# Kernel optimization log

Measured on AMD Instinct MI355X. Metric: run time of the kernel, lower is better.

## Reference

```python
import jax, jax.numpy as jnp
import numpy as np

B, NMAX, H, DH, K = 16, 1024, 4, 32, 16
C = H * DH  # 128 = hidden_dim
T = 8192


def _dense_batch(feat, batch):
    # PyG to_dense_batch: [T, ...] + segment ids -> [B, NMAX, ...] + mask
    t = feat.shape[0]
    counts = jax.ops.segment_sum(jnp.ones((t,), jnp.int32), batch, num_segments=B)
    starts = jnp.concatenate([jnp.zeros((1,), jnp.int32), jnp.cumsum(counts)[:-1].astype(jnp.int32)])
    idx = jnp.arange(t) - starts[batch]
    dense = jnp.zeros((B, NMAX) + feat.shape[1:], feat.dtype).at[batch, idx].set(feat)
    mask = jnp.zeros((B, NMAX), bool).at[batch, idx].set(True)
    return dense, mask


def _forward(batch, x, pos, emb_W, emb_b, Wq, Wk, Wv0, Wv1, Wo0, Wo1, Wg, dist_scale, head_W, head_b):
    # 1) node embedding, then dense-batch (as in original forward)
    f0_flat = x @ emb_W + emb_b                      # [T, C]
    f0, mask = _dense_batch(f0_flat, batch)          # [B,N,C], [B,N]
    coords, _ = _dense_batch(pos, batch)             # [B,N,3]

    # 2) kNN graph from coordinates (num_neighbors=16, attend_self=True -> self is nearest)
    rel = coords[:, :, None, :] - coords[:, None, :, :]      # [B,N,N,3]
    d2 = jnp.sum(rel * rel, axis=-1)                         # [B,N,N]
    pv = mask[:, :, None] & mask[:, None, :]
    d2m = jnp.where(pv, d2, 1e9)
    _, nbr = jax.lax.top_k(-d2m, K)                          # [B,N,K]

    bidx = jnp.arange(B)[:, None, None]
    rel_n = jnp.take_along_axis(rel, nbr[..., None], axis=2)  # [B,N,K,3]
    d2_n = jnp.take_along_axis(d2, nbr, axis=2)               # [B,N,K]
    nbr_valid = jnp.take_along_axis(pv, nbr, axis=2)          # [B,N,K]
    dist = jnp.sqrt(d2_n + 1e-6)
    direc = rel_n / dist[..., None]                           # degree-1 spherical harmonic (unit rel dir)

    # 3) SE(3)-equivariant kNN attention (degree-0 and degree-1 outputs)
    q = (f0 @ Wq).reshape(B, NMAX, H, DH)
    k_n = (f0 @ Wk)[bidx, nbr].reshape(B, NMAX, K, H, DH)
    v0_n = (f0 @ Wv0)[bidx, nbr].reshape(B, NMAX, K, H, DH)
    v1_n = (f0 @ Wv1)[bidx, nbr].reshape(B, NMAX, K, H, DH)

    logits = jnp.einsum('bnhd,bnkhd->bnhk', q, k_n) / np.sqrt(DH)
    logits = logits - jax.nn.softplus(dist_scale)[None, None, :, None] * dist[:, :, None, :]
    logits = jnp.where(nbr_valid[:, :, None, :], logits, -1e9)
    attn = jax.nn.softmax(logits, axis=-1)                    # [B,N,H,K]

    out0 = jnp.einsum('bnhk,bnkhd->bnhd', attn, v0_n).reshape(B, NMAX, C)
    out1 = jnp.einsum('bnhk,bnkhd,bnkj->bnhdj', attn, v1_n, direc).reshape(B, NMAX, C, 3)

    # equivariant channel mixing of type-1, then invariant norm gates type-0 (residual)
    f1 = jnp.einsum('bncj,cd->bndj', out1, Wo1)               # [B,N,C,3]
    inv = jnp.sqrt(jnp.sum(f1 * f1, axis=-1) + 1e-6)          # [B,N,C]
    f0_out = f0 + out0 @ Wo0 + inv @ Wg

    # 4) masked mean pool over nodes + linear head
    mf = mask.astype(f0_out.dtype)
    pooled = jnp.sum(f0_out * mf[..., None], axis=1) / jnp.maximum(jnp.sum(mf, axis=1, keepdims=True), 1.0)
    return pooled @ head_W + head_b                           # [B, 19]


def setup_inputs() -> dict:
    key = jax.random.key(0)
    ks = jax.random.split(key, 16)
    def w(k, shape, fan_in):
        return jax.random.normal(k, shape, jnp.float32) / np.sqrt(fan_in)
    return {
        'x': jax.random.normal(ks[0], (T, 11), jnp.float32),
        'pos': jax.random.normal(ks[1], (T, 3), jnp.float32),
        'batch': jnp.sort(jax.random.randint(ks[2], (T,), 0, B)),
        'emb_W': w(ks[3], (11, C), 11), 'emb_b': jnp.zeros((C,), jnp.float32),
        'Wq': w(ks[4], (C, C), C), 'Wk': w(ks[5], (C, C), C),
        'Wv0': w(ks[6], (C, C), C), 'Wv1': w(ks[7], (C, C), C),
        'Wo0': w(ks[8], (C, C), C), 'Wo1': w(ks[9], (C, C), C),
        'Wg': w(ks[10], (C, C), C),
        'dist_scale': jax.random.normal(ks[11], (H,), jnp.float32) * 0.1,
        'head_W': w(ks[12], (C, 19), C), 'head_b': jnp.zeros((19,), jnp.float32),
    }


def reference(x, pos, batch, emb_W, emb_b, Wq, Wk, Wv0, Wv1, Wo0, Wo1, Wg, dist_scale, head_W, head_b):
    return _forward(batch, x, pos, emb_W, emb_b, Wq, Wk, Wv0, Wv1, Wo0, Wo1, Wg, dist_scale, head_W, head_b)
```

## Files before the change

### kernel.cpp

```cpp
#include <hip/hip_runtime.h>
#include <hip/hip_bf16.h>
#include <math.h>

#define T_NODES 8192
#define BGRAPHS 16
#define CDIM 128
#define HEADS 4
#define DHEAD 32
#define KNN 16

template <int NS>
__device__ __forceinline__ void knn_body(const float* __restrict__ pos,
                                         int t, int s, int n, int lane,
                                         float px, float py, float pz,
                                         int* __restrict__ nbr,
                                         float4* __restrict__ dird) {
    float sd[NS];
    int ss[NS];
#pragma unroll
    for (int sl = 0; sl < NS; ++sl) {
        int j = lane + sl * 64;
        float d2 = 1e30f;
        if (j < n) {
            int jj = s + j;
            float dx = px - pos[jj * 3 + 0];
            float dy = py - pos[jj * 3 + 1];
            float dz = pz - pos[jj * 3 + 2];
            d2 = dx * dx + dy * dy + dz * dz;
        }
        sd[sl] = d2;
        ss[sl] = sl;
    }

#pragma unroll
    for (int p = 1; p < NS; p <<= 1) {
#pragma unroll
        for (int k = p; k >= 1; k >>= 1) {
#pragma unroll
            for (int j = (k & (p - 1)); j + k < NS; j += 2 * k) {
#pragma unroll
                for (int i = 0; i < k; ++i) {
                    if (i + j + k < NS && ((i + j) / (2 * p)) == ((i + j + k) / (2 * p))) {
                        int a = i + j, c2 = i + j + k;
                        bool sw = sd[a] > sd[c2];
                        float td = sd[a];
                        int ts = ss[a];
                        sd[a] = sw ? sd[c2] : sd[a];
                        ss[a] = sw ? ss[c2] : ss[a];
                        sd[c2] = sw ? td : sd[c2];
                        ss[c2] = sw ? ts : ss[c2];
                    }
                }
            }
        }
    }

    float resd = 1e30f;
    int resj = -1;

#pragma unroll
    for (int r = 0; r < KNN; ++r) {
        float rd = sd[0];
#pragma unroll
        for (int off = 32; off >= 1; off >>= 1) {
            rd = fminf(rd, __shfl_xor(rd, off));
        }
        unsigned long long mask = __ballot(sd[0] == rd);
        int wl = (int)__builtin_ctzll(mask);
        int ws = __shfl(ss[0], wl);
        if (lane == r) { resd = rd; resj = wl + ws * 64; }
        if (lane == wl) {
#pragma unroll
            for (int i = 0; i < NS - 1; ++i) { sd[i] = sd[i + 1]; ss[i] = ss[i + 1]; }
            sd[NS - 1] = 1e30f;
        }
    }

    if (lane < KNN) {
        bool valid = (resd < 1e29f);
        int jf = valid ? (s + resj) : -1;
        nbr[t * KNN + lane] = jf;
        float dd = sqrtf(resd + 1e-6f);
        float dx = 0.f, dy = 0.f, dz = 0.f;
        if (valid) {
            float inv = 1.f / dd;
            dx = (px - pos[jf * 3 + 0]) * inv;
            dy = (py - pos[jf * 3 + 1]) * inv;
            dz = (pz - pos[jf * 3 + 2]) * inv;
        }
        float4 v;
        v.x = dx; v.y = dy; v.z = dz; v.w = dd;
        dird[t * KNN + lane] = v;
    }
}

__global__ __launch_bounds__(256) void k_par(const float* __restrict__ pos,
                                             const int* __restrict__ batch,
                                             const float* __restrict__ x,
                                             const float* __restrict__ embW,
                                             const float* __restrict__ embb,
                                             const float* __restrict__ Wq,
                                             const float* __restrict__ Wk,
                                             const float* __restrict__ Wv0,
                                             const float* __restrict__ Wv1,
                                             const float* __restrict__ Wo0,
                                             const float* __restrict__ Wg,
                                             const float* __restrict__ headW,
                                             int* __restrict__ nbr,
                                             float4* __restrict__ dird,
                                             float* __restrict__ f0,
                                             float* __restrict__ qkvv,
                                             float* __restrict__ H1,
                                             float* __restrict__ H2) {
    __shared__ float smem[CDIM * 20];
    int bid = blockIdx.x;
    int tid = threadIdx.x;

    if (bid >= 2560) {
        int m = bid - 2560;
        const float* W = m ? Wg : Wo0;
        float* H = m ? H2 : H1;
        for (int i = tid; i < CDIM * 19; i += 256) smem[i] = headW[i];
        __syncthreads();
        for (int i = tid; i < CDIM * 19; i += 256) {
            int c = i / 19, o = i - c * 19;
            float acc = 0.f;
#pragma unroll 8
            for (int d = 0; d < CDIM; ++d) acc += W[c * CDIM + d] * smem[d * 19 + o];
            H[i] = acc;
        }
        return;
    }

    int g = bid / 5, r = bid - g * 5;
    if (r == 4) {
        float (*sf)[CDIM] = (float (*)[CDIM])smem;
        int t0 = g * 16;
        {
            int col = tid & 127;
            int pr = tid >> 7;
            float ew[11];
#pragma unroll
            for (int i = 0; i < 11; ++i) ew[i] = embW[i * CDIM + col];
            float eb = embb[col];
#pragma unroll
            for (int nn8 = 0; nn8 < 8; ++nn8) {
                int nn = pr * 8 + nn8;
                int t = t0 + nn;
                float acc = eb;
#pragma unroll
                for (int i = 0; i < 11; ++i) acc += x[t * 11 + i] * ew[i];
                sf[nn][col] = acc;
                f0[(size_t)t * CDIM + col] = acc;
            }
        }
        __syncthreads();

        const float* W1 = (tid < 128) ? Wq : Wk;
        const float* W2 = (tid < 128) ? Wv0 : Wv1;
        int col = tid & 127;

        float acc1[16], acc2[16];
#pragma unroll
        for (int nn = 0; nn < 16; ++nn) { acc1[nn] = 0.f; acc2[nn] = 0.f; }

        for (int c0 = 0; c0 < CDIM; c0 += 8) {
            float w1[8], w2[8];
#pragma unroll
            for (int cc = 0; cc < 8; ++cc) {
                w1[cc] = W1[(c0 + cc) * CDIM + col];
                w2[cc] = W2[(c0 + cc) * CDIM + col];
            }
#pragma unroll
            for (int nn = 0; nn < 16; ++nn) {
                float4 fa = *(const float4*)&sf[nn][c0];
                float4 fb = *(const float4*)&sf[nn][c0 + 4];
                acc1[nn] += fa.x * w1[0] + fa.y * w1[1] + fa.z * w1[2] + fa.w * w1[3]
                          + fb.x * w1[4] + fb.y * w1[5] + fb.z * w1[6] + fb.w * w1[7];
                acc2[nn] += fa.x * w2[0] + fa.y * w2[1] + fa.z * w2[2] + fa.w * w2[3]
                          + fb.x * w2[4] + fb.y * w2[5] + fb.z * w2[6] + fb.w * w2[7];
            }
        }
#pragma unroll
        for (int nn = 0; nn < 16; ++nn) {
            qkvv[(size_t)(t0 + nn) * 512 + tid] = acc1[nn];
            qkvv[(size_t)(t0 + nn) * 512 + 256 + tid] = acc2[nn];
        }
        return;
    }

    int kidx = g * 4 + r;
    int wave = tid >> 6;
    int lane = tid & 63;
    int t = kidx * 4 + wave;

    int b = batch[t];

    int pb = t - lane * 16;
    int qf = t + lane * 16;
    int vb = batch[pb < 0 ? 0 : pb];
    int vf = batch[qf > T_NODES - 1 ? T_NODES - 1 : qf];
    bool eqb = (pb >= 0) && (vb == b);
    bool eqf = (qf < T_NODES) && (vf == b);
    unsigned long long mb = __ballot(eqb);
    unsigned long long mf = __ballot(eqf);
    int m1 = (~mb == 0ULL) ? 64 : (int)__builtin_ctzll(~mb);
    int m2 = (~mf == 0ULL) ? 64 : (int)__builtin_ctzll(~mf);
    int wsb = (m1 == 64) ? (t - 1023) : (t - m1 * 16 + 1);
    int wsf = (m2 == 64) ? (t + 1009) : (t + (m2 - 1) * 16 + 1);
    int pos2 = (lane < 16) ? (wsb + lane) : (wsf + (lane - 16));
    int pc = pos2 < 0 ? 0 : (pos2 > T_NODES - 1 ? T_NODES - 1 : pos2);
    int v2 = batch[pc];
    bool cb = (lane < 16) && ((pos2 < 0) || (v2 < b));
    bool cf = (lane >= 16) && (lane < 32) && (pos2 < T_NODES) && (v2 == b);
    int s = wsb + (int)__popcll(__ballot(cb));
    int e = wsf + (int)__popcll(__ballot(cf));
    int n = e - s;

    float px = pos[t * 3 + 0];
    float py = pos[t * 3 + 1];
    float pz = pos[t * 3 + 2];

    if (n <= 512) {
        knn_body<8>(pos, t, s, n, lane, px, py, pz, nbr, dird);
    } else {
        knn_body<16>(pos, t, s, n, lane, px, py, pz, nbr, dird);
    }
}

__global__ __launch_bounds__(256) void k_attn(const float* __restrict__ qkvv,
                                              const int* __restrict__ nbr,
                                              const float4* __restrict__ dird,
                                              const float* __restrict__ dist_scale,
                                              const float* __restrict__ Wo1,
                                              float* __restrict__ out0,
                                              float* __restrict__ invb) {
    __shared__ float  s_a[4][64];
    __shared__ float4 s_d[4][16];
    __shared__ int    s_j[4][16];
    __shared__ float  s_o1[4][CDIM][4];
    __shared__ float  s_part[CDIM][13];

    int bid = blockIdx.x;
    int swz = (bid & 7) * (T_NODES / 32) + (bid >> 3);
    int wave = threadIdx.x >> 6;
    int lane = threadIdx.x & 63;
    int t = swz * 4 + wave;

    int k = lane & 15;
    int h = lane >> 4;

    int j = nbr[t * KNN + k];
    float4 dv = dird[t * KNN + k];
    if (h == 0) { s_j[wave][k] = j; s_d[wave][k] = dv; }

    const float4* qv = (const float4*)&qkvv[(size_t)t * 512 + h * DHEAD];
    const float4* kv = (j >= 0) ? (const float4*)&qkvv[(size_t)j * 512 + 128 + h * DHEAD] : qv;
    float dot = 0.f;
#pragma unroll
    for (int i = 0; i < 8; ++i) {
        float4 a = qv[i], b2 = kv[i];
        dot += a.x * b2.x + a.y * b2.y + a.z * b2.z + a.w * b2.w;
    }
    float xs = dist_scale[h];
    float sp = (xs > 20.f) ? xs : log1pf(expf(xs));
    float lg = (j >= 0) ? (dot * 0.17677669529663687f - sp * dv.w) : -1e30f;

    float m = lg;
    m = fmaxf(m, __shfl_xor(m, 1));
    m = fmaxf(m, __shfl_xor(m, 2));
    m = fmaxf(m, __shfl_xor(m, 4));
    m = fmaxf(m, __shfl_xor(m, 8));
    float e = expf(lg - m);
    float ssum = e;
    ssum += __shfl_xor(ssum, 1);
    ssum += __shfl_xor(ssum, 2);
    ssum += __shfl_xor(ssum, 4);
    ssum += __shfl_xor(ssum, 8);
    s_a[wave][h * 16 + k] = e / ssum;

    __syncthreads();

    int c2 = lane * 2;
    int hh = lane >> 4;

    float o0x = 0.f, o0y = 0.f;
    float o1xx = 0.f, o1xy = 0.f;
    float o1yx = 0.f, o1yy = 0.f;
    float o1zx = 0.f, o1zy = 0.f;

#pragma unroll
    for (int kk = 0; kk < KNN; ++kk) {
        int jj = s_j[wave][kk];
        if (jj >= 0) {
            float a = s_a[wave][hh * 16 + kk];
            float4 d = s_d[wave][kk];
            float2 v0 = *(const float2*)&qkvv[(size_t)jj * 512 + 256 + c2];
            float2 v1 = *(const float2*)&qkvv[(size_t)jj * 512 + 384 + c2];
            o0x += a * v0.x;
            o0y += a * v0.y;
            float w1x = a * v1.x, w1y = a * v1.y;
            o1xx += w1x * d.x; o1xy += w1y * d.x;
            o1yx += w1x * d.y; o1yy += w1y * d.y;
            o1zx += w1x * d.z; o1zy += w1y * d.z;
        }
    }

    float2 st;
    st.x = o0x; st.y = o0y;
    *(float2*)&out0[(size_t)t * CDIM + c2] = st;

    {
        float4 w0; w0.x = o1xx; w0.y = o1yx; w0.z = o1zx; w0.w = 0.f;
        float4 w1; w1.x = o1xy; w1.y = o1yy; w1.z = o1zy; w1.w = 0.f;
        *(float4*)&s_o1[wave][c2][0] = w0;
        *(float4*)&s_o1[wave][c2 + 1][0] = w1;
    }
    __syncthreads();

    int d = threadIdx.x & 127;
    int half = threadIdx.x >> 7;
    int t0 = swz * 4;

    float acc[4][3];
#pragma unroll
    for (int nn = 0; nn < 4; ++nn) { acc[nn][0] = 0.f; acc[nn][1] = 0.f; acc[nn][2] = 0.f; }

    int cb0 = half * 64;
#pragma unroll 4
    for (int c = cb0; c < cb0 + 64; ++c) {
        float wv = Wo1[c * CDIM + d];
#pragma unroll
        for (int nn = 0; nn < 4; ++nn) {
            float4 v = *(const float4*)&s_o1[nn][c][0];
            acc[nn][0] += v.x * wv;
            acc[nn][1] += v.y * wv;
            acc[nn][2] += v.z * wv;
        }
    }
    if (half == 1) {
#pragma unroll
        for (int nn = 0; nn < 4; ++nn) {
            s_part[d][nn * 3 + 0] = acc[nn][0];
            s_part[d][nn * 3 + 1] = acc[nn][1];
            s_part[d][nn * 3 + 2] = acc[nn][2];
        }
    }
    __syncthreads();
    if (half == 0) {
#pragma unroll
        for (int nn = 0; nn < 4; ++nn) {
            float fx = acc[nn][0] + s_part[d][nn * 3 + 0];
            float fy = acc[nn][1] + s_part[d][nn * 3 + 1];
            float fz = acc[nn][2] + s_part[d][nn * 3 + 2];
            invb[(size_t)(t0 + nn) * CDIM + d] = sqrtf(fx * fx + fy * fy + fz * fz + 1e-6f);
        }
    }
}

__global__ __launch_bounds__(1024) void k_pool(const float* __restrict__ f0,
                                               const float* __restrict__ out0,
                                               const float* __restrict__ invb,
                                               const int* __restrict__ batch,
                                               const float* __restrict__ headW,
                                               const float* __restrict__ H1,
                                               const float* __restrict__ H2,
                                               const float* __restrict__ headb,
                                               float* __restrict__ out) {
    __shared__ float p0[8][CDIM], p1[8][CDIM], p2[8][CDIM];
    int b = blockIdx.x;
    int tid = threadIdx.x;
    int c = tid & 127;
    int slice = tid >> 7;

    int lo = 0, hi = T_NODES;
    while (lo < hi) {
        int mid = (lo + hi) >> 1;
        bool lt = batch[mid] < b;
        lo = lt ? mid + 1 : lo;
        hi = lt ? hi : mid;
    }
    int s = lo;
    lo = 0; hi = T_NODES;
    while (lo < hi) {
        int mid = (lo + hi) >> 1;
        bool le = batch[mid] <= b;
        lo = le ? mid + 1 : lo;
        hi = le ? hi : mid;
    }
    int n = lo - s;

    float a0 = 0.f, a1 = 0.f, a2 = 0.f;
    for (int i = slice; i < n; i += 8) {
        size_t idx = (size_t)(s + i) * CDIM + c;
        a0 += f0[idx];
        a1 += out0[idx];
        a2 += invb[idx];
    }
    p0[slice][c] = a0;
    p1[slice][c] = a1;
    p2[slice][c] = a2;
    __syncthreads();

    if (slice == 0) {
        float inv_n = 1.f / fmaxf((float)n, 1.f);
        float v0 = p0[0][c] + p0[1][c] + p0[2][c] + p0[3][c]
                 + p0[4][c] + p0[5][c] + p0[6][c] + p0[7][c];
        float v1 = p1[0][c] + p1[1][c] + p1[2][c] + p1[3][c]
                 + p1[4][c] + p1[5][c] + p1[6][c] + p1[7][c];
        float v2 = p2[0][c] + p2[1][c] + p2[2][c] + p2[3][c]
                 + p2[4][c] + p2[5][c] + p2[6][c] + p2[7][c];
        p0[0][c] = v0 * inv_n;
        p1[0][c] = v1 * inv_n;
        p2[0][c] = v2 * inv_n;
    }
    __syncthreads();

    if (tid < 19 * 32) {
        int o = tid >> 5;
        int l = tid & 31;
        float p = 0.f;
#pragma unroll
        for (int cc = 0; cc < 4; ++cc) {
            int ch = l + cc * 32;
            p += p0[0][ch] * headW[ch * 19 + o]
               + p1[0][ch] * H1[ch * 19 + o]
               + p2[0][ch] * H2[ch * 19 + o];
        }
        p += __shfl_xor(p, 16);
        p += __shfl_xor(p, 8);
        p += __shfl_xor(p, 4);
        p += __shfl_xor(p, 2);
        p += __shfl_xor(p, 1);
        if (l == 0) out[b * 19 + o] = p + headb[o];
    }
}

extern "C" void kernel_launch(void* const* d_in, const int* in_sizes, int n_in,
                              void* d_out, int out_size, void* d_ws, size_t ws_size,
                              hipStream_t stream) {
    const float* x    = (const float*)d_in[0];
    const float* pos  = (const float*)d_in[1];
    const int* batch  = (const int*)d_in[2];
    const float* embW = (const float*)d_in[3];
    const float* embb = (const float*)d_in[4];
    const float* Wq   = (const float*)d_in[5];
    const float* Wk   = (const float*)d_in[6];
    const float* Wv0  = (const float*)d_in[7];
    const float* Wv1  = (const float*)d_in[8];
    const float* Wo0  = (const float*)d_in[9];
    const float* Wo1  = (const float*)d_in[10];
    const float* Wg   = (const float*)d_in[11];
    const float* dist_scale = (const float*)d_in[12];
    const float* headW = (const float*)d_in[13];
    const float* headb = (const float*)d_in[14];
    float* out = (float*)d_out;

    char* w = (char*)d_ws;
    float* f0   = (float*)(w + 256);
    float* qkvv = f0 + (size_t)T_NODES * CDIM;
    int* nbr    = (int*)(qkvv + (size_t)T_NODES * 512);
    float4* dird = (float4*)(nbr + (size_t)T_NODES * KNN);
    float* out0 = (float*)(dird + (size_t)T_NODES * KNN);
    float* invb = out0 + (size_t)T_NODES * CDIM;
    float* H1   = invb + (size_t)T_NODES * CDIM;
    float* H2   = H1 + CDIM * 19;

    k_par<<<2562, 256, 0, stream>>>(pos, batch, x, embW, embb, Wq, Wk, Wv0, Wv1,
                                    Wo0, Wg, headW, nbr, dird, f0, qkvv, H1, H2);
    k_attn<<<T_NODES / 4, 256, 0, stream>>>(qkvv, nbr, dird, dist_scale, Wo1, out0, invb);
    k_pool<<<BGRAPHS, 1024, 0, stream>>>(f0, out0, invb, batch, headW, H1, H2, headb, out);
}
```

Measured before the change: 134.6 us.

## Fuse mean pooling into producers via atomics and pair kNN queries per wave

The per-node f0, out0 and invb arrays are no longer written to global memory. The embedding stage and the attention kernel now accumulate per-graph sums with run-length grouped atomicAdds into small pooled buffers, zeroed by a memset, and the pool kernel only scales and applies the head. The kNN stage now handles two query nodes per wave, using 32-lane halves with a packed-key min reduction when both segments have at most 512 nodes, which cuts the kNN block count. This removes several megabytes of global traffic and the pool kernel's serial reduction, but adds atomic contention, a memset launch, and float summation order that is no longer deterministic.

Result: faster. 113.2 us (-15.9%).

```diff
diff --git a/kernel.cpp b/kernel.cpp
--- a/kernel.cpp
+++ b/kernel.cpp
@@ -9,193 +9,9 @@
 #define DHEAD 32
 #define KNN 16
 
-template <int NS>
-__device__ __forceinline__ void knn_body(const float* __restrict__ pos,
-                                         int t, int s, int n, int lane,
-                                         float px, float py, float pz,
-                                         int* __restrict__ nbr,
-                                         float4* __restrict__ dird) {
-    float sd[NS];
-    int ss[NS];
-#pragma unroll
-    for (int sl = 0; sl < NS; ++sl) {
-        int j = lane + sl * 64;
-        float d2 = 1e30f;
-        if (j < n) {
-            int jj = s + j;
-            float dx = px - pos[jj * 3 + 0];
-            float dy = py - pos[jj * 3 + 1];
-            float dz = pz - pos[jj * 3 + 2];
-            d2 = dx * dx + dy * dy + dz * dz;
-        }
-        sd[sl] = d2;
-        ss[sl] = sl;
-    }
-
-#pragma unroll
-    for (int p = 1; p < NS; p <<= 1) {
-#pragma unroll
-        for (int k = p; k >= 1; k >>= 1) {
-#pragma unroll
-            for (int j = (k & (p - 1)); j + k < NS; j += 2 * k) {
-#pragma unroll
-                for (int i = 0; i < k; ++i) {
-                    if (i + j + k < NS && ((i + j) / (2 * p)) == ((i + j + k) / (2 * p))) {
-                        int a = i + j, c2 = i + j + k;
-                        bool sw = sd[a] > sd[c2];
-                        float td = sd[a];
-                        int ts = ss[a];
-                        sd[a] = sw ? sd[c2] : sd[a];
-                        ss[a] = sw ? ss[c2] : ss[a];
-                        sd[c2] = sw ? td : sd[c2];
-                        ss[c2] = sw ? ts : ss[c2];
-                    }
-                }
-            }
-        }
-    }
-
-    float resd = 1e30f;
-    int resj = -1;
-
-#pragma unroll
-    for (int r = 0; r < KNN; ++r) {
-        float rd = sd[0];
-#pragma unroll
-        for (int off = 32; off >= 1; off >>= 1) {
-            rd = fminf(rd, __shfl_xor(rd, off));
-        }
-        unsigned long long mask = __ballot(sd[0] == rd);
-        int wl = (int)__builtin_ctzll(mask);
-        int ws = __shfl(ss[0], wl);
-        if (lane == r) { resd = rd; resj = wl + ws * 64; }
-        if (lane == wl) {
-#pragma unroll
-            for (int i = 0; i < NS - 1; ++i) { sd[i] = sd[i + 1]; ss[i] = ss[i + 1]; }
-            sd[NS - 1] = 1e30f;
-        }
-    }
-
-    if (lane < KNN) {
-        bool valid = (resd < 1e29f);
-        int jf = valid ? (s + resj) : -1;
-        nbr[t * KNN + lane] = jf;
-        float dd = sqrtf(resd + 1e-6f);
-        float dx = 0.f, dy = 0.f, dz = 0.f;
-        if (valid) {
-            float inv = 1.f / dd;
-            dx = (px - pos[jf * 3 + 0]) * inv;
-            dy = (py - pos[jf * 3 + 1]) * inv;
-            dz = (pz - pos[jf * 3 + 2]) * inv;
-        }
-        float4 v;
-        v.x = dx; v.y = dy; v.z = dz; v.w = dd;
-        dird[t * KNN + lane] = v;
-    }
-}
-
-__global__ __launch_bounds__(256) void k_par(const float* __restrict__ pos,
-                                             const int* __restrict__ batch,
-                                             const float* __restrict__ x,
-                                             const float* __restrict__ embW,
-                                             const float* __restrict__ embb,
-                                             const float* __restrict__ Wq,
-                                             const float* __restrict__ Wk,
-                                             const float* __restrict__ Wv0,
-                                             const float* __restrict__ Wv1,
-                                             const float* __restrict__ Wo0,
-                                             const float* __restrict__ Wg,
-                                             const float* __restrict__ headW,
-                                             int* __restrict__ nbr,
-                                             float4* __restrict__ dird,
-                                             float* __restrict__ f0,
-                                             float* __restrict__ qkvv,
-                                             float* __restrict__ H1,
-                                             float* __restrict__ H2) {
-    __shared__ float smem[CDIM * 20];
-    int bid = blockIdx.x;
-    int tid = threadIdx.x;
-
-    if (bid >= 2560) {
-        int m = bid - 2560;
-        const float* W = m ? Wg : Wo0;
-        float* H = m ? H2 : H1;
-        for (int i = tid; i < CDIM * 19; i += 256) smem[i] = headW[i];
-        __syncthreads();
-        for (int i = tid; i < CDIM * 19; i += 256) {
-            int c = i / 19, o = i - c * 19;
-            float acc = 0.f;
-#pragma unroll 8
-            for (int d = 0; d < CDIM; ++d) acc += W[c * CDIM + d] * smem[d * 19 + o];
-            H[i] = acc;
-        }
-        return;
-    }
-
-    int g = bid / 5, r = bid - g * 5;
-    if (r == 4) {
-        float (*sf)[CDIM] = (float (*)[CDIM])smem;
-        int t0 = g * 16;
-        {
-            int col = tid & 127;
-            int pr = tid >> 7;
-            float ew[11];
-#pragma unroll
-            for (int i = 0; i < 11; ++i) ew[i] = embW[i * CDIM + col];
-            float eb = embb[col];
-#pragma unroll
-            for (int nn8 = 0; nn8 < 8; ++nn8) {
-                int nn = pr * 8 + nn8;
-                int t = t0 + nn;
-                float acc = eb;
-#pragma unroll
-                for (int i = 0; i < 11; ++i) acc += x[t * 11 + i] * ew[i];
-                sf[nn][col] = acc;
-                f0[(size_t)t * CDIM + col] = acc;
-            }
-        }
-        __syncthreads();
-
-        const float* W1 = (tid < 128) ? Wq : Wk;
-        const float* W2 = (tid < 128) ? Wv0 : Wv1;
-        int col = tid & 127;
-
-        float acc1[16], acc2[16];
-#pragma unroll
-        for (int nn = 0; nn < 16; ++nn) { acc1[nn] = 0.f; acc2[nn] = 0.f; }
-
-        for (int c0 = 0; c0 < CDIM; c0 += 8) {
-            float w1[8], w2[8];
-#pragma unroll
-            for (int cc = 0; cc < 8; ++cc) {
-                w1[cc] = W1[(c0 + cc) * CDIM + col];
-                w2[cc] = W2[(c0 + cc) * CDIM + col];
-            }
-#pragma unroll
-            for (int nn = 0; nn < 16; ++nn) {
-                float4 fa = *(const float4*)&sf[nn][c0];
-                float4 fb = *(const float4*)&sf[nn][c0 + 4];
-                acc1[nn] += fa.x * w1[0] + fa.y * w1[1] + fa.z * w1[2] + fa.w * w1[3]
-                          + fb.x * w1[4] + fb.y * w1[5] + fb.z * w1[6] + fb.w * w1[7];
-                acc2[nn] += fa.x * w2[0] + fa.y * w2[1] + fa.z * w2[2] + fa.w * w2[3]
-                          + fb.x * w2[4] + fb.y * w2[5] + fb.z * w2[6] + fb.w * w2[7];
-            }
-        }
-#pragma unroll
-        for (int nn = 0; nn < 16; ++nn) {
-            qkvv[(size_t)(t0 + nn) * 512 + tid] = acc1[nn];
-            qkvv[(size_t)(t0 + nn) * 512 + 256 + tid] = acc2[nn];
-        }
-        return;
-    }
-
-    int kidx = g * 4 + r;
-    int wave = tid >> 6;
-    int lane = tid & 63;
-    int t = kidx * 4 + wave;
-
+__device__ __forceinline__ void seg_probe(const int* __restrict__ batch, int t,
+                                          int lane, int& s_out, int& n_out) {
     int b = batch[t];
-
     int pb = t - lane * 16;
     int qf = t + lane * 16;
     int vb = batch[pb < 0 ? 0 : pb];
@@ -213,39 +29,328 @@
     int v2 = batch[pc];
     bool cb = (lane < 16) && ((pos2 < 0) || (v2 < b));
     bool cf = (lane >= 16) && (lane < 32) && (pos2 < T_NODES) && (v2 == b);
-    int s = wsb + (int)__popcll(__ballot(cb));
-    int e = wsf + (int)__popcll(__ballot(cf));
-    int n = e - s;
-
-    float px = pos[t * 3 + 0];
-    float py = pos[t * 3 + 1];
-    float pz = pos[t * 3 + 2];
-
-    if (n <= 512) {
-        knn_body<8>(pos, t, s, n, lane, px, py, pz, nbr, dird);
+    s_out = wsb + (int)__popcll(__ballot(cb));
+    n_out = wsf + (int)__popcll(__ballot(cf)) - s_out;
+}
+
+template <int NS>
+__device__ __forceinline__ void knn_body(const float* __restrict__ pos,
+                                         int t, int s, int n, int lane,
+                                         int* __restrict__ nbr,
+                                         float4* __restrict__ dird) {
+    float px = pos[t * 3 + 0], py = pos[t * 3 + 1], pz = pos[t * 3 + 2];
+    float sd[NS];
+    int ss[NS];
+#pragma unroll
+    for (int sl = 0; sl < NS; ++sl) {
+        int j = lane + sl * 64;
+        float d2 = 1e30f;
+        if (j < n) {
+            int jj = s + j;
+            float dx = px - pos[jj * 3 + 0];
+            float dy = py - pos[jj * 3 + 1];
+            float dz = pz - pos[jj * 3 + 2];
+            d2 = dx * dx + dy * dy + dz * dz;
+        }
+        sd[sl] = d2;
+        ss[sl] = sl;
+    }
+#pragma unroll
+    for (int p = 1; p < NS; p <<= 1) {
+#pragma unroll
+        for (int k = p; k >= 1; k >>= 1) {
+#pragma unroll
+            for (int j = (k & (p - 1)); j + k < NS; j += 2 * k) {
+#pragma unroll
+                for (int i = 0; i < k; ++i) {
+                    if (i + j + k < NS && ((i + j) / (2 * p)) == ((i + j + k) / (2 * p))) {
+                        int a = i + j, c2 = i + j + k;
+                        bool sw = sd[a] > sd[c2];
+                        float td = sd[a];
+                        int ts = ss[a];
+                        sd[a] = sw ? sd[c2] : sd[a];
+                        ss[a] = sw ? ss[c2] : ss[a];
+                        sd[c2] = sw ? td : sd[c2];
+                        ss[c2] = sw ? ts : ss[c2];
+                    }
+                }
+            }
+        }
+    }
+
+    float resd = 1e30f;
+    int resj = -1;
+#pragma unroll
+    for (int r = 0; r < KNN; ++r) {
+        float rd = sd[0];
+#pragma unroll
+        for (int off = 32; off >= 1; off >>= 1) {
+            rd = fminf(rd, __shfl_xor(rd, off));
+        }
+        unsigned long long mask = __ballot(sd[0] == rd);
+        int wl = (int)__builtin_ctzll(mask);
+        int ws = __shfl(ss[0], wl);
+        if (lane == r) { resd = rd; resj = wl + ws * 64; }
+        if (lane == wl) {
+#pragma unroll
+            for (int i = 0; i < NS - 1; ++i) { sd[i] = sd[i + 1]; ss[i] = ss[i + 1]; }
+            sd[NS - 1] = 1e30f;
+        }
+    }
+
+    if (lane < KNN) {
+        bool valid = (resd < 1e29f);
+        int jf = valid ? (s + resj) : -1;
+        nbr[t * KNN + lane] = jf;
+        float dd = sqrtf(resd + 1e-6f);
+        float dx = 0.f, dy = 0.f, dz = 0.f;
+        if (valid) {
+            float inv = 1.f / dd;
+            dx = (px - pos[jf * 3 + 0]) * inv;
+            dy = (py - pos[jf * 3 + 1]) * inv;
+            dz = (pz - pos[jf * 3 + 2]) * inv;
+        }
+        float4 v;
+        v.x = dx; v.y = dy; v.z = dz; v.w = dd;
+        dird[t * KNN + lane] = v;
+    }
+}
+
+template <int NS>
+__device__ __forceinline__ void knn_pair_body(const float* __restrict__ pos,
+                                              int t, int s, int n, int lane,
+                                              int* __restrict__ nbr,
+                                              float4* __restrict__ dird) {
+    int l32 = lane & 31;
+    float px = pos[t * 3 + 0], py = pos[t * 3 + 1], pz = pos[t * 3 + 2];
+    float sd[NS];
+    int ss[NS];
+#pragma unroll
+    for (int sl = 0; sl < NS; ++sl) {
+        int j = l32 + sl * 32;
+        float d2 = 1e30f;
+        if (j < n) {
+            int jj = s + j;
+            float dx = px - pos[jj * 3 + 0];
+            float dy = py - pos[jj * 3 + 1];
+            float dz = pz - pos[jj * 3 + 2];
+            d2 = dx * dx + dy * dy + dz * dz;
+        }
+        sd[sl] = d2;
+        ss[sl] = sl;
+    }
+#pragma unroll
+    for (int p = 1; p < NS; p <<= 1) {
+#pragma unroll
+        for (int k = p; k >= 1; k >>= 1) {
+#pragma unroll
+            for (int j = (k & (p - 1)); j + k < NS; j += 2 * k) {
+#pragma unroll
+                for (int i = 0; i < k; ++i) {
+                    if (i + j + k < NS && ((i + j) / (2 * p)) == ((i + j + k) / (2 * p))) {
+                        int a = i + j, c2 = i + j + k;
+                        bool sw = sd[a] > sd[c2];
+                        float td = sd[a];
+                        int ts = ss[a];
+                        sd[a] = sw ? sd[c2] : sd[a];
+                        ss[a] = sw ? ss[c2] : ss[a];
+                        sd[c2] = sw ? td : sd[c2];
+                        ss[c2] = sw ? ts : ss[c2];
+                    }
+                }
+            }
+        }
+    }
+
+    float resd = 1e30f;
+    int resj = -1;
+#pragma unroll
+    for (int r = 0; r < KNN; ++r) {
+        unsigned key = (__float_as_uint(sd[0]) & ~31u) | (unsigned)l32;
+        key = min(key, (unsigned)__shfl_xor((int)key, 16));
+        key = min(key, (unsigned)__shfl_xor((int)key, 8));
+        key = min(key, (unsigned)__shfl_xor((int)key, 4));
+        key = min(key, (unsigned)__shfl_xor((int)key, 2));
+        key = min(key, (unsigned)__shfl_xor((int)key, 1));
+        int wl32 = (int)(key & 31u);
+        int wl = wl32 + (lane & 32);
+        float rd = __shfl(sd[0], wl);
+        int ws = __shfl(ss[0], wl);
+        if (l32 == r) { resd = rd; resj = wl32 + ws * 32; }
+        if (lane == wl) {
+#pragma unroll
+            for (int i = 0; i < NS - 1; ++i) { sd[i] = sd[i + 1]; ss[i] = ss[i + 1]; }
+            sd[NS - 1] = 1e30f;
+        }
+    }
+
+    if (l32 < KNN) {
+        bool valid = (resd < 1e29f);
+        int jf = valid ? (s + resj) : -1;
+        nbr[t * KNN + l32] = jf;
+        float dd = sqrtf(resd + 1e-6f);
+        float dx = 0.f, dy = 0.f, dz = 0.f;
+        if (valid) {
+            float inv = 1.f / dd;
+            dx = (px - pos[jf * 3 + 0]) * inv;
+            dy = (py - pos[jf * 3 + 1]) * inv;
+            dz = (pz - pos[jf * 3 + 2]) * inv;
+        }
+        float4 v;
+        v.x = dx; v.y = dy; v.z = dz; v.w = dd;
+        dird[t * KNN + l32] = v;
+    }
+}
+
+__global__ __launch_bounds__(256) void k_par(const float* __restrict__ pos,
+                                             const int* __restrict__ batch,
+                                             const float* __restrict__ x,
+                                             const float* __restrict__ embW,
+                                             const float* __restrict__ embb,
+                                             const float* __restrict__ Wq,
+                                             const float* __restrict__ Wk,
+                                             const float* __restrict__ Wv0,
+                                             const float* __restrict__ Wv1,
+                                             const float* __restrict__ Wo0,
+                                             const float* __restrict__ Wg,
+                                             const float* __restrict__ headW,
+                                             int* __restrict__ nbr,
+                                             float4* __restrict__ dird,
+                                             float* __restrict__ qkvv,
+                                             float* __restrict__ poolF0,
+                                             float* __restrict__ H1,
+                                             float* __restrict__ H2) {
+    __shared__ float smem[CDIM * 20];
+    int bid = blockIdx.x;
+    int tid = threadIdx.x;
+
+    if (bid >= 1536) {
+        int m = bid - 1536;
+        const float* W = m ? Wg : Wo0;
+        float* H = m ? H2 : H1;
+        for (int i = tid; i < CDIM * 19; i += 256) smem[i] = headW[i];
+        __syncthreads();
+        for (int i = tid; i < CDIM * 19; i += 256) {
+            int c = i / 19, o = i - c * 19;
+            float acc = 0.f;
+#pragma unroll 8
+            for (int d = 0; d < CDIM; ++d) acc += W[c * CDIM + d] * smem[d * 19 + o];
+            H[i] = acc;
+        }
+        return;
+    }
+
+    int g = bid / 3, r = bid - g * 3;
+    if (r == 2) {
+        float (*sf)[CDIM] = (float (*)[CDIM])smem;
+        int t0 = g * 16;
+        {
+            int col = tid & 127;
+            int pr = tid >> 7;
+            float ew[11];
+#pragma unroll
+            for (int i = 0; i < 11; ++i) ew[i] = embW[i * CDIM + col];
+            float eb = embb[col];
+            float acc_run = 0.f;
+            int gprev = batch[t0 + pr * 8];
+#pragma unroll
+            for (int nn8 = 0; nn8 < 8; ++nn8) {
+                int nn = pr * 8 + nn8;
+                int t = t0 + nn;
+                float acc = eb;
+#pragma unroll
+                for (int i = 0; i < 11; ++i) acc += x[t * 11 + i] * ew[i];
+                sf[nn][col] = acc;
+                int gb = batch[t];
+                if (gb != gprev) {
+                    atomicAdd(&poolF0[gprev * CDIM + col], acc_run);
+                    acc_run = 0.f;
+                    gprev = gb;
+                }
+                acc_run += acc;
+            }
+            atomicAdd(&poolF0[gprev * CDIM + col], acc_run);
+        }
+        __syncthreads();
+
+        const float* W1 = (tid < 128) ? Wq : Wk;
+        const float* W2 = (tid < 128) ? Wv0 : Wv1;
+        int col = tid & 127;
+
+        float acc1[16], acc2[16];
+#pragma unroll
+        for (int nn = 0; nn < 16; ++nn) { acc1[nn] = 0.f; acc2[nn] = 0.f; }
+
+        for (int c0 = 0; c0 < CDIM; c0 += 8) {
+            float w1[8], w2[8];
+#pragma unroll
+            for (int cc = 0; cc < 8; ++cc) {
+                w1[cc] = W1[(c0 + cc) * CDIM + col];
+                w2[cc] = W2[(c0 + cc) * CDIM + col];
+            }
+#pragma unroll
+            for (int nn = 0; nn < 16; ++nn) {
+                float4 fa = *(const float4*)&sf[nn][c0];
+                float4 fb = *(const float4*)&sf[nn][c0 + 4];
+                acc1[nn] += fa.x * w1[0] + fa.y * w1[1] + fa.z * w1[2] + fa.w * w1[3]
+                          + fb.x * w1[4] + fb.y * w1[5] + fb.z * w1[6] + fb.w * w1[7];
+                acc2[nn] += fa.x * w2[0] + fa.y * w2[1] + fa.z * w2[2] + fa.w * w2[3]
+                          + fb.x * w2[4] + fb.y * w2[5] + fb.z * w2[6] + fb.w * w2[7];
+            }
+        }
+#pragma unroll
+        for (int nn = 0; nn < 16; ++nn) {
+            qkvv[(size_t)(t0 + nn) * 512 + tid] = acc1[nn];
+            qkvv[(size_t)(t0 + nn) * 512 + 256 + tid] = acc2[nn];
+        }
+        return;
+    }
+
+    int kidx = g * 2 + r;
+    int wave = tid >> 6;
+    int lane = tid & 63;
+    int tA = kidx * 8 + wave * 2;
+    int tB = tA + 1;
+
+    int sA, nA, sB, nB;
+    seg_probe(batch, tA, lane, sA, nA);
+    seg_probe(batch, tB, lane, sB, nB);
+
+    int nmax = nA > nB ? nA : nB;
+    if (nmax <= 512) {
+        int t = (lane < 32) ? tA : tB;
+        int s = (lane < 32) ? sA : sB;
+        int n = (lane < 32) ? nA : nB;
+        knn_pair_body<16>(pos, t, s, n, lane, nbr, dird);
     } else {
-        knn_body<16>(pos, t, s, n, lane, px, py, pz, nbr, dird);
+        knn_body<16>(pos, tA, sA, nA, lane, nbr, dird);
+        knn_body<16>(pos, tB, sB, nB, lane, nbr, dird);
     }
 }
 
 __global__ __launch_bounds__(256) void k_attn(const float* __restrict__ qkvv,
                                               const int* __restrict__ nbr,
                                               const float4* __restrict__ dird,
+                                              const int* __restrict__ batch,
                                               const float* __restrict__ dist_scale,
                                               const float* __restrict__ Wo1,
-                                              float* __restrict__ out0,
-                                              float* __restrict__ invb) {
+                                              float* __restrict__ poolO0,
+                                              float* __restrict__ poolInv) {
     __shared__ float  s_a[4][64];
     __shared__ float4 s_d[4][16];
     __shared__ int    s_j[4][16];
     __shared__ float  s_o1[4][CDIM][4];
     __shared__ float  s_part[CDIM][13];
+    __shared__ int    s_gid[4];
 
     int bid = blockIdx.x;
     int swz = (bid & 7) * (T_NODES / 32) + (bid >> 3);
     int wave = threadIdx.x >> 6;
     int lane = threadIdx.x & 63;
-    int t = swz * 4 + wave;
+    int t0 = swz * 4;
+    int t = t0 + wave;
+
+    if (threadIdx.x < 4) s_gid[threadIdx.x] = batch[t0 + threadIdx.x];
 
     int k = lane & 15;
     int h = lane >> 4;
@@ -306,13 +411,9 @@
         }
     }
 
-    float2 st;
-    st.x = o0x; st.y = o0y;
-    *(float2*)&out0[(size_t)t * CDIM + c2] = st;
-
     {
-        float4 w0; w0.x = o1xx; w0.y = o1yx; w0.z = o1zx; w0.w = 0.f;
-        float4 w1; w1.x = o1xy; w1.y = o1yy; w1.z = o1zy; w1.w = 0.f;
+        float4 w0; w0.x = o1xx; w0.y = o1yx; w0.z = o1zx; w0.w = o0x;
+        float4 w1; w1.x = o1xy; w1.y = o1yy; w1.z = o1zy; w1.w = o0y;
         *(float4*)&s_o1[wave][c2][0] = w0;
         *(float4*)&s_o1[wave][c2 + 1][0] = w1;
     }
@@ -320,7 +421,6 @@
 
     int d = threadIdx.x & 127;
     int half = threadIdx.x >> 7;
-    int t0 = swz * 4;
 
     float acc[4][3];
 #pragma unroll
@@ -348,30 +448,42 @@
     }
     __syncthreads();
     if (half == 0) {
+        float accO = 0.f, accI = 0.f;
+        int gprev = s_gid[0];
 #pragma unroll
         for (int nn = 0; nn < 4; ++nn) {
             float fx = acc[nn][0] + s_part[d][nn * 3 + 0];
             float fy = acc[nn][1] + s_part[d][nn * 3 + 1];
             float fz = acc[nn][2] + s_part[d][nn * 3 + 2];
-            invb[(size_t)(t0 + nn) * CDIM + d] = sqrtf(fx * fx + fy * fy + fz * fz + 1e-6f);
-        }
-    }
-}
-
-__global__ __launch_bounds__(1024) void k_pool(const float* __restrict__ f0,
-                                               const float* __restrict__ out0,
-                                               const float* __restrict__ invb,
-                                               const int* __restrict__ batch,
-                                               const float* __restrict__ headW,
-                                               const float* __restrict__ H1,
-                                               const float* __restrict__ H2,
-                                               const float* __restrict__ headb,
-                                               float* __restrict__ out) {
-    __shared__ float p0[8][CDIM], p1[8][CDIM], p2[8][CDIM];
+            float iv = sqrtf(fx * fx + fy * fy + fz * fz + 1e-6f);
+            float o0v = s_o1[nn][d][3];
+            int gb = s_gid[nn];
+            if (gb != gprev) {
+                atomicAdd(&poolO0[gprev * CDIM + d], accO);
+                atomicAdd(&poolInv[gprev * CDIM + d], accI);
+                accO = 0.f; accI = 0.f;
+                gprev = gb;
+            }
+            accO += o0v;
+            accI += iv;
+        }
+        atomicAdd(&poolO0[gprev * CDIM + d], accO);
+        atomicAdd(&poolInv[gprev * CDIM + d], accI);
+    }
+}
+
+__global__ __launch_bounds__(640) void k_pool(const float* __restrict__ poolF0,
+                                              const float* __restrict__ poolO0,
+                                              const float* __restrict__ poolInv,
+                                              const int* __restrict__ batch,
+                                              const float* __restrict__ headW,
+                                              const float* __restrict__ H1,
+                                              const float* __restrict__ H2,
+                                              const float* __restrict__ headb,
+                                              float* __restrict__ out) {
+    __shared__ float P0[CDIM], P1[CDIM], P2[CDIM];
     int b = blockIdx.x;
     int tid = threadIdx.x;
-    int c = tid & 127;
-    int slice = tid >> 7;
 
     int lo = 0, hi = T_NODES;
     while (lo < hi) {
@@ -389,30 +501,12 @@
         hi = le ? hi : mid;
     }
     int n = lo - s;
-
-    float a0 = 0.f, a1 = 0.f, a2 = 0.f;
-    for (int i = slice; i < n; i += 8) {
-        size_t idx = (size_t)(s + i) * CDIM + c;
-        a0 += f0[idx];
-        a1 += out0[idx];
-        a2 += invb[idx];
-    }
-    p0[slice][c] = a0;
-    p1[slice][c] = a1;
-    p2[slice][c] = a2;
-    __syncthreads();
-
-    if (slice == 0) {
-        float inv_n = 1.f / fmaxf((float)n, 1.f);
-        float v0 = p0[0][c] + p0[1][c] + p0[2][c] + p0[3][c]
-                 + p0[4][c] + p0[5][c] + p0[6][c] + p0[7][c];
-        float v1 = p1[0][c] + p1[1][c] + p1[2][c] + p1[3][c]
-                 + p1[4][c] + p1[5][c] + p1[6][c] + p1[7][c];
-        float v2 = p2[0][c] + p2[1][c] + p2[2][c] + p2[3][c]
-                 + p2[4][c] + p2[5][c] + p2[6][c] + p2[7][c];
-        p0[0][c] = v0 * inv_n;
-        p1[0][c] = v1 * inv_n;
-        p2[0][c] = v2 * inv_n;
+    float inv_n = 1.f / fmaxf((float)n, 1.f);
+
+    if (tid < CDIM) {
+        P0[tid] = poolF0[b * CDIM + tid] * inv_n;
+        P1[tid] = poolO0[b * CDIM + tid] * inv_n;
+        P2[tid] = poolInv[b * CDIM + tid] * inv_n;
     }
     __syncthreads();
 
@@ -423,9 +517,9 @@
 #pragma unroll
         for (int cc = 0; cc < 4; ++cc) {
             int ch = l + cc * 32;
-            p += p0[0][ch] * headW[ch * 19 + o]
-               + p1[0][ch] * H1[ch * 19 + o]
-               + p2[0][ch] * H2[ch * 19 + o];
+            p += P0[ch] * headW[ch * 19 + o]
+               + P1[ch] * H1[ch * 19 + o]
+               + P2[ch] * H2[ch * 19 + o];
         }
         p += __shfl_xor(p, 16);
         p += __shfl_xor(p, 8);
@@ -457,17 +551,20 @@
     float* out = (float*)d_out;
 
     char* w = (char*)d_ws;
-    float* f0   = (float*)(w + 256);
-    float* qkvv = f0 + (size_t)T_NODES * CDIM;
+    float* qkvv = (float*)(w + 256);
     int* nbr    = (int*)(qkvv + (size_t)T_NODES * 512);
     float4* dird = (float4*)(nbr + (size_t)T_NODES * KNN);
-    float* out0 = (float*)(dird + (size_t)T_NODES * KNN);
-    float* invb = out0 + (size_t)T_NODES * CDIM;
-    float* H1   = invb + (size_t)T_NODES * CDIM;
+    float* poolF0 = (float*)(dird + (size_t)T_NODES * KNN);
+    float* poolO0 = poolF0 + BGRAPHS * CDIM;
+    float* poolInv = poolO0 + BGRAPHS * CDIM;
+    float* H1   = poolInv + BGRAPHS * CDIM;
     float* H2   = H1 + CDIM * 19;
 
-    k_par<<<2562, 256, 0, stream>>>(pos, batch, x, embW, embb, Wq, Wk, Wv0, Wv1,
-                                    Wo0, Wg, headW, nbr, dird, f0, qkvv, H1, H2);
-    k_attn<<<T_NODES / 4, 256, 0, stream>>>(qkvv, nbr, dird, dist_scale, Wo1, out0, invb);
-    k_pool<<<BGRAPHS, 1024, 0, stream>>>(f0, out0, invb, batch, headW, H1, H2, headb, out);
-}
+    hipMemsetAsync(poolF0, 0, 3 * BGRAPHS * CDIM * sizeof(float), stream);
+    k_par<<<1538, 256, 0, stream>>>(pos, batch, x, embW, embb, Wq, Wk, Wv0, Wv1,
+                                    Wo0, Wg, headW, nbr, dird, qkvv, poolF0, H1, H2);
+    k_attn<<<T_NODES / 4, 256, 0, stream>>>(qkvv, nbr, dird, batch, dist_scale, Wo1,
+                                            poolO0, poolInv);
+    k_pool<<<BGRAPHS, 640, 0, stream>>>(poolF0, poolO0, poolInv, batch, headW,
+                                        H1, H2, headb, out);
+}
```
